# Performance work log

Hardware: AMD Instinct MI355X
Metric: run time of the kernel (lower is better)

The kernel has to match this reference:

```python
import jax, jax.numpy as jnp
import numpy as np

N_EXPERTS = 16
DS_DIM = 3

def _conv2d(x, w):
    # x: [B,C,H,W], w: [O,I,kH,kW], VALID, stride 1
    return jax.lax.conv_general_dilated(x, w, (1, 1), 'VALID',
                                        dimension_numbers=('NCHW', 'OIHW', 'NCHW'))

def _maxpool2(x):
    return jax.lax.reduce_window(x, -jnp.inf, jax.lax.max,
                                 (1, 1, 2, 2), (1, 1, 2, 2), 'VALID')

def _forward(x, conv1_w, conv1_b, conv2_w, conv2_b,
             fc1_w, fc1_b, fc2_w, fc2_b, fc3_w, fc3_b,
             fc4_w, fc4_b, fc5_w, fc5_b, B_mats, C_mats, x_tar):
    bsz = x.shape[0]
    img = x[:, DS_DIM:].reshape(bsz, 1, 64, 64)
    h = _maxpool2(jax.nn.relu(_conv2d(img, conv1_w) + conv1_b[None, :, None, None]))
    h = _maxpool2(jax.nn.relu(_conv2d(h, conv2_w) + conv2_b[None, :, None, None]))
    h = h.reshape(bsz, -1)                      # [B, 1690]
    h = jnp.concatenate([h, x[:, :DS_DIM]], axis=1)  # [B, 1693]
    h = jax.nn.relu(h @ fc1_w.T + fc1_b)
    h = jax.nn.relu(h @ fc2_w.T + fc2_b)
    h = jax.nn.relu(h @ fc3_w.T + fc3_b)
    h = jax.nn.relu(h @ fc4_w.T + fc4_b)
    w_all = jax.nn.softmax(h @ fc5_w.T + fc5_b, axis=1)   # [B, N]
    A = B_mats + C_mats                          # [N, d, d]
    diff = x_tar - x[:, :DS_DIM]                 # [B, d]
    # torch: sum_i w[:,i,None] * (A_i @ diff.T).T == einsum over experts
    s_all = jnp.einsum('bn,nij,bj->bi', w_all, A, diff)
    return s_all


def setup_inputs() -> dict:
    key = jax.random.key(0)
    ks = jax.random.split(key, 20)
    rn = lambda k, shp, s: jax.random.normal(k, shp, dtype=jnp.float32) * s
    d = {}
    d['x'] = rn(ks[0], (8192, 4099), 1.0)
    d['conv1_w'] = rn(ks[1], (5, 1, 5, 5), 0.2)
    d['conv1_b'] = rn(ks[2], (5,), 0.05)
    d['conv2_w'] = rn(ks[3], (10, 5, 5, 5), 0.09)
    d['conv2_b'] = rn(ks[4], (10,), 0.05)
    d['fc1_w'] = rn(ks[5], (512, 1693), 1.0 / np.sqrt(1693))
    d['fc1_b'] = rn(ks[6], (512,), 0.02)
    d['fc2_w'] = rn(ks[7], (256, 512), 1.0 / np.sqrt(512))
    d['fc2_b'] = rn(ks[8], (256,), 0.02)
    d['fc3_w'] = rn(ks[9], (128, 256), 1.0 / np.sqrt(256))
    d['fc3_b'] = rn(ks[10], (128,), 0.02)
    d['fc4_w'] = rn(ks[11], (64, 128), 1.0 / np.sqrt(128))
    d['fc4_b'] = rn(ks[12], (64,), 0.02)
    d['fc5_w'] = rn(ks[13], (N_EXPERTS, 64), 1.0 / np.sqrt(64))
    d['fc5_b'] = rn(ks[14], (N_EXPERTS,), 0.02)
    # geotorch constrains B to PSD and C to skew-symmetric; build such mats
    G = rn(ks[15], (N_EXPERTS, DS_DIM, DS_DIM), 0.5)
    d['B_mats'] = jnp.einsum('nij,nkj->nik', G, G)        # PSD
    S = rn(ks[16], (N_EXPERTS, DS_DIM, DS_DIM), 0.5)
    d['C_mats'] = S - jnp.swapaxes(S, 1, 2)               # skew
    d['x_tar'] = jnp.zeros((1, DS_DIM), dtype=jnp.float32)
    return d


def reference(x, conv1_w, conv1_b, conv2_w, conv2_b,
              fc1_w, fc1_b, fc2_w, fc2_b, fc3_w, fc3_b,
              fc4_w, fc4_b, fc5_w, fc5_b, B_mats, C_mats, x_tar):
    return _forward(x, conv1_w, conv1_b, conv2_w, conv2_b,
                    fc1_w, fc1_b, fc2_w, fc2_b, fc3_w, fc3_b,
                    fc4_w, fc4_b, fc5_w, fc5_b, B_mats, C_mats, x_tar)
```

## Files before the change

kernel.cpp:

```cpp
#include <hip/hip_runtime.h>
#include <hip/hip_bf16.h>
#include <hip/hip_fp16.h>
#include <math.h>

#define XW 4099
#define DSD 3
#define BSZ 8192
#define KP1 1696

typedef __attribute__((ext_vector_type(8))) _Float16 f16x8;
typedef __attribute__((ext_vector_type(4))) float    f32x4;

static __device__ __forceinline__ short f2h(float f) {
    union { _Float16 h; short s; } u;
    u.h = (_Float16)f;
    return u.s;
}

__global__ __launch_bounds__(256) void cvt_f16_pad(
    const float* __restrict__ src, short* __restrict__ dst,
    int N, int K, int Kp)
{
    const int tot = N * Kp;
    for (int i = blockIdx.x * 256 + threadIdx.x; i < tot; i += gridDim.x * 256) {
        const int n = i / Kp, k = i % Kp;
        dst[i] = (k < K) ? f2h(src[(size_t)n * K + k]) : (short)0;
    }
}

__global__ __launch_bounds__(256, 4) void conv_fused(
    const float* __restrict__ x,
    const float* __restrict__ w1, const float* __restrict__ b1,
    const float* __restrict__ w2, const float* __restrict__ b2,
    short* __restrict__ act1)
{
    __shared__ __align__(16) char smem0[64 * 68 * 4];
    float     (*img)[68]  = (float(*)[68])smem0;
    _Float16  (*w2f)[224] = (_Float16(*)[224])smem0;

    __shared__ __align__(16) _Float16  h1[30][30][8];
    __shared__ __align__(16) float     cw1[5][28];
    __shared__ float cb1[5];
    __shared__ float cb2s[16];
    __shared__ __align__(16) int kofft[28];

    const int b = blockIdx.x;
    const int t = threadIdx.x;

    const float* xr = x + (size_t)b * XW + DSD;
    #pragma unroll
    for (int i = 0; i < 16; ++i) {
        const int idx = t + 256 * i;
        img[idx >> 6][idx & 63] = xr[idx];
    }
    {
        uint4* h1z = (uint4*)&h1[0][0][0];
        const uint4 z4 = {0u, 0u, 0u, 0u};
        #pragma unroll
        for (int i = 0; i < 4; ++i) {
            const int idx = t + 256 * i;
            if (idx < 900) h1z[idx] = z4;
        }
    }
    if (t < 140) { const int c = t / 28, k = t % 28; cw1[c][k] = (k < 25) ? w1[c * 25 + k] : 0.f; }
    if (t >= 144 && t < 149) cb1[t - 144] = b1[t - 144];
    if (t >= 160 && t < 176) cb2s[t - 160] = (t - 160 < 10) ? b2[t - 160] : 0.f;
    if (t >= 192 && t < 220) {
        const int p = t - 192;
        kofft[p] = (p < 25) ? (p / 5) * 480 + (p % 5) * 16 : 0;
    }
    __syncthreads();

    if (t < 225) {
        const int ty = t / 15, tx = t % 15;
        const int y0 = 4 * ty, x0 = 4 * tx;
        f32x4 pv[8][2];
        #pragma unroll
        for (int r = 0; r < 8; ++r) {
            pv[r][0] = *(const f32x4*)&img[y0 + r][x0];
            pv[r][1] = *(const f32x4*)&img[y0 + r][x0 + 4];
        }
        asm volatile("" :
            "+v"(pv[0][0]), "+v"(pv[0][1]), "+v"(pv[1][0]), "+v"(pv[1][1]),
            "+v"(pv[2][0]), "+v"(pv[2][1]), "+v"(pv[3][0]), "+v"(pv[3][1]),
            "+v"(pv[4][0]), "+v"(pv[4][1]), "+v"(pv[5][0]), "+v"(pv[5][1]),
            "+v"(pv[6][0]), "+v"(pv[6][1]), "+v"(pv[7][0]), "+v"(pv[7][1]));
        #pragma unroll 1
        for (int c = 0; c < 5; ++c) {
            f32x4 wv4[7];
            #pragma unroll
            for (int i = 0; i < 7; ++i) wv4[i] = *(const f32x4*)&cw1[c][4 * i];
            const float bias = cb1[c];
            float acc[4][4];
            #pragma unroll
            for (int cy = 0; cy < 4; ++cy)
                #pragma unroll
                for (int cx = 0; cx < 4; ++cx) acc[cy][cx] = bias;
            #pragma unroll
            for (int ky = 0; ky < 5; ++ky)
                #pragma unroll
                for (int kx = 0; kx < 5; ++kx) {
                    const int kk = ky * 5 + kx;
                    const float wv = wv4[kk >> 2][kk & 3];
                    #pragma unroll
                    for (int cy = 0; cy < 4; ++cy)
                        #pragma unroll
                        for (int cx = 0; cx < 4; ++cx) {
                            const int px = cx + kx;
                            acc[cy][cx] += pv[cy + ky][px >> 2][px & 3] * wv;
                        }
                }
            #pragma unroll
            for (int sy = 0; sy < 2; ++sy)
                #pragma unroll
                for (int sx = 0; sx < 2; ++sx) {
                    const float m = fmaxf(
                        fmaxf(acc[2 * sy][2 * sx],     acc[2 * sy][2 * sx + 1]),
                        fmaxf(acc[2 * sy + 1][2 * sx], acc[2 * sy + 1][2 * sx + 1]));
                    h1[2 * ty + sy][2 * tx + sx][c] = (_Float16)fmaxf(m, 0.f);
                }
        }
    }
    __syncthreads();

    for (int i = t; i < 448; i += 256) {
        const int wc = i / 28, wp = i % 28;
        f16x8 cell;
        #pragma unroll
        for (int ic = 0; ic < 8; ++ic) cell[ic] = (_Float16)0.f;
        if (wc < 10 && wp < 25) {
            #pragma unroll
            for (int ic = 0; ic < 5; ++ic)
                cell[ic] = (_Float16)w2[(wc * 5 + ic) * 25 + wp];
        }
        *(f16x8*)&w2f[wc][wp * 8] = cell;
    }
    __syncthreads();

    short* outr = act1 + (size_t)b * KP1;
    {
        const int wv_ = t >> 6, lane = t & 63;
        const int lr = lane & 15, kg = lane >> 4;
        const float bias2 = cb2s[lr];
        const int qa = lr & 3;
        const int wa_off = lr >> 2;

        int bases[11];
        #pragma unroll
        for (int u = 0; u < 11; ++u) {
            const int tt = u * 4 + wv_;
            int w_A = tt * 4 + wa_off;
            w_A = (w_A < 169) ? w_A : 168;
            const int Y = (w_A * 5042) >> 16;
            const int X = w_A - Y * 13;
            bases[u] = (2 * Y + (qa & 1)) * 480 + (2 * X + (qa >> 1)) * 16;
        }

        f32x4 acc[11];
        #pragma unroll
        for (int u = 0; u < 11; ++u) acc[u] = (f32x4){0.f, 0.f, 0.f, 0.f};

        const char* h1p = (const char*)&h1[0][0][0];

        #pragma unroll 1
        for (int s = 0; s < 7; ++s) {
            const int koffp = kofft[s * 4 + kg];
            const f16x8 bfs = *(const f16x8*)&w2f[lr][s * 32 + kg * 8];
            #pragma unroll
            for (int u = 0; u < 11; ++u) {
                const f16x8 af = *(const f16x8*)(h1p + (bases[u] + koffp));
                acc[u] = __builtin_amdgcn_mfma_f32_16x16x32_f16(af, bfs, acc[u], 0, 0, 0);
            }
        }

        #pragma unroll
        for (int u = 0; u < 11; ++u) {
            const int tt = u * 4 + wv_;
            const int w_C = tt * 4 + kg;
            if (lr < 10 && w_C < 169) {
                const float m = fmaxf(fmaxf(acc[u][0], acc[u][1]), fmaxf(acc[u][2], acc[u][3]));
                outr[lr * 169 + w_C] = f2h(fmaxf(m + bias2, 0.f));
            }
        }
    }
    if (t < DSD)           outr[1690 + t] = f2h(x[(size_t)b * XW + t]);
    if (t >= DSD && t < 6) outr[1690 + t] = 0;
}

template <int RELU, int OUTH>
__global__ __launch_bounds__(256) void mfma_fc(
    const short* __restrict__ A,
    const short* __restrict__ W,
    const float* __restrict__ bias,
    void* __restrict__ Cout,
    int N, int Kp)
{
    __shared__ __align__(16) short As[64][40];
    __shared__ __align__(16) short Ws[64][40];

    const int tid  = threadIdx.x;
    const int m0   = blockIdx.y * 64;
    const int n0   = blockIdx.x * 64;
    const int wv   = tid >> 6, lane = tid & 63;
    const int rm   = (wv >> 1) * 32, rn = (wv & 1) * 32;
    const int lr   = lane & 15, kg = lane >> 4;
    const int sr   = tid >> 2, sc = (tid & 3) * 8;

    f32x4 acc[2][2];
    #pragma unroll
    for (int i = 0; i < 2; ++i)
        #pragma unroll
        for (int j = 0; j < 2; ++j)
            #pragma unroll
            for (int q = 0; q < 4; ++q) acc[i][j][q] = 0.f;

    for (int k0 = 0; k0 < Kp; k0 += 32) {
        *(uint4*)&As[sr][sc] = *(const uint4*)&A[(size_t)(m0 + sr) * Kp + k0 + sc];
        *(uint4*)&Ws[sr][sc] = *(const uint4*)&W[(size_t)(n0 + sr) * Kp + k0 + sc];
        __syncthreads();
        f16x8 aF[2], bF[2];
        #pragma unroll
        for (int mi = 0; mi < 2; ++mi) aF[mi] = *(const f16x8*)&As[rm + mi * 16 + lr][kg * 8];
        #pragma unroll
        for (int nj = 0; nj < 2; ++nj) bF[nj] = *(const f16x8*)&Ws[rn + nj * 16 + lr][kg * 8];
        #pragma unroll
        for (int mi = 0; mi < 2; ++mi)
            #pragma unroll
            for (int nj = 0; nj < 2; ++nj)
                acc[mi][nj] = __builtin_amdgcn_mfma_f32_16x16x32_f16(
                    aF[mi], bF[nj], acc[mi][nj], 0, 0, 0);
        __syncthreads();
    }

    #pragma unroll
    for (int mi = 0; mi < 2; ++mi)
        #pragma unroll
        for (int nj = 0; nj < 2; ++nj) {
            const int col  = n0 + rn + nj * 16 + lr;
            const int rowb = m0 + rm + mi * 16 + kg * 4;
            const float bv = bias[col];
            #pragma unroll
            for (int q = 0; q < 4; ++q) {
                float v = acc[mi][nj][q] + bv;
                if (RELU) v = fmaxf(v, 0.f);
                if (OUTH) ((short*)Cout)[(size_t)(rowb + q) * N + col] = f2h(v);
                else      ((float*)Cout)[(size_t)(rowb + q) * N + col] = v;
            }
        }
}

__global__ __launch_bounds__(256) void head_kernel(
    const float* __restrict__ act5, const float* __restrict__ w5,
    const float* __restrict__ b5, const float* __restrict__ Bm,
    const float* __restrict__ Cm, const float* __restrict__ x,
    const float* __restrict__ x_tar, float* __restrict__ out)
{
    __shared__ float sw[16 * 64];
    __shared__ float sb[16];
    __shared__ float sA[16 * 9];
    __shared__ float st[3];
    const int t = threadIdx.x;
    for (int i = t; i < 1024; i += 256) sw[i] = w5[i];
    if (t < 16)  sb[t] = b5[t];
    if (t < 144) sA[t] = Bm[t] + Cm[t];
    if (t < 3)   st[t] = x_tar[t];
    __syncthreads();

    const int b = blockIdx.x * 256 + t;
    float h[64];
    const float* ar = act5 + (size_t)b * 64;
    #pragma unroll
    for (int i = 0; i < 64; ++i) h[i] = ar[i];

    float logit[16];
    float mx = -1e30f;
    #pragma unroll
    for (int n = 0; n < 16; ++n) {
        float s = sb[n];
        const float* wr = sw + n * 64;
        #pragma unroll
        for (int i = 0; i < 64; ++i) s += h[i] * wr[i];
        logit[n] = s;
        mx = fmaxf(mx, s);
    }
    float sum = 0.f;
    #pragma unroll
    for (int n = 0; n < 16; ++n) { logit[n] = __expf(logit[n] - mx); sum += logit[n]; }
    const float inv = 1.f / sum;

    const float d0 = st[0] - x[(size_t)b * XW + 0];
    const float d1 = st[1] - x[(size_t)b * XW + 1];
    const float d2 = st[2] - x[(size_t)b * XW + 2];
    float s0 = 0.f, s1 = 0.f, s2 = 0.f;
    #pragma unroll
    for (int n = 0; n < 16; ++n) {
        const float w = logit[n] * inv;
        const float* An = sA + n * 9;
        s0 += w * (An[0] * d0 + An[1] * d1 + An[2] * d2);
        s1 += w * (An[3] * d0 + An[4] * d1 + An[5] * d2);
        s2 += w * (An[6] * d0 + An[7] * d1 + An[8] * d2);
    }
    out[(size_t)b * 3 + 0] = s0;
    out[(size_t)b * 3 + 1] = s1;
    out[(size_t)b * 3 + 2] = s2;
}

extern "C" void kernel_launch(void* const* d_in, const int* in_sizes, int n_in,
                              void* d_out, int out_size, void* d_ws, size_t ws_size,
                              hipStream_t stream) {
    const float* x       = (const float*)d_in[0];
    const float* conv1_w = (const float*)d_in[1];
    const float* conv1_b = (const float*)d_in[2];
    const float* conv2_w = (const float*)d_in[3];
    const float* conv2_b = (const float*)d_in[4];
    const float* fc1_w   = (const float*)d_in[5];
    const float* fc1_b   = (const float*)d_in[6];
    const float* fc2_w   = (const float*)d_in[7];
    const float* fc2_b   = (const float*)d_in[8];
    const float* fc3_w   = (const float*)d_in[9];
    const float* fc3_b   = (const float*)d_in[10];
    const float* fc4_w   = (const float*)d_in[11];
    const float* fc4_b   = (const float*)d_in[12];
    const float* fc5_w   = (const float*)d_in[13];
    const float* fc5_b   = (const float*)d_in[14];
    const float* B_mats  = (const float*)d_in[15];
    const float* C_mats  = (const float*)d_in[16];
    const float* x_tar   = (const float*)d_in[17];
    float* out = (float*)d_out;

    char* p = (char*)d_ws;
    short* act1 = (short*)p;  p += (size_t)BSZ * KP1 * 2;
    short* act2 = (short*)p;  p += (size_t)BSZ * 512 * 2;
    short* act3 = (short*)p;  p += (size_t)BSZ * 256 * 2;
    short* act4 = (short*)p;  p += (size_t)BSZ * 128 * 2;
    float* act5 = (float*)p;  p += (size_t)BSZ * 64 * 4;
    short* w1h  = (short*)p;  p += (size_t)512 * KP1 * 2;
    short* w2h  = (short*)p;  p += (size_t)256 * 512 * 2;
    short* w3h  = (short*)p;  p += (size_t)128 * 256 * 2;
    short* w4h  = (short*)p;  p += (size_t)64 * 128 * 2;

    cvt_f16_pad<<<1024, 256, 0, stream>>>(fc1_w, w1h, 512, 1693, KP1);
    cvt_f16_pad<<<256,  256, 0, stream>>>(fc2_w, w2h, 256, 512, 512);
    cvt_f16_pad<<<64,   256, 0, stream>>>(fc3_w, w3h, 128, 256, 256);
    cvt_f16_pad<<<16,   256, 0, stream>>>(fc4_w, w4h, 64, 128, 128);

    conv_fused<<<BSZ, 256, 0, stream>>>(x, conv1_w, conv1_b, conv2_w, conv2_b, act1);

    mfma_fc<1, 1><<<dim3(512 / 64, BSZ / 64), 256, 0, stream>>>(act1, w1h, fc1_b, act2, 512, KP1);
    mfma_fc<1, 1><<<dim3(256 / 64, BSZ / 64), 256, 0, stream>>>(act2, w2h, fc2_b, act3, 256, 512);
    mfma_fc<1, 1><<<dim3(128 / 64, BSZ / 64), 256, 0, stream>>>(act3, w3h, fc3_b, act4, 128, 256);
    mfma_fc<1, 0><<<dim3(64 / 64,  BSZ / 64), 256, 0, stream>>>(act4, w4h, fc4_b, act5, 64, 128);

    head_kernel<<<BSZ / 256, 256, 0, stream>>>(act5, fc5_w, fc5_b, B_mats, C_mats, x, x_tar, out);
}
```

Before: 218.2 us.

## Split conv1 into half-row passes and use 128-row tiles for fc1 GEMM

```diff
diff --git a/kernel.cpp b/kernel.cpp
--- a/kernel.cpp
+++ b/kernel.cpp
@@ -39,8 +39,6 @@
     _Float16  (*w2f)[224] = (_Float16(*)[224])smem0;
 
     __shared__ __align__(16) _Float16  h1[30][30][8];
-    __shared__ __align__(16) float     cw1[5][28];
-    __shared__ float cb1[5];
     __shared__ float cb2s[16];
     __shared__ __align__(16) int kofft[28];
 
@@ -62,8 +60,6 @@
             if (idx < 900) h1z[idx] = z4;
         }
     }
-    if (t < 140) { const int c = t / 28, k = t % 28; cw1[c][k] = (k < 25) ? w1[c * 25 + k] : 0.f; }
-    if (t >= 144 && t < 149) cb1[t - 144] = b1[t - 144];
     if (t >= 160 && t < 176) cb2s[t - 160] = (t - 160 < 10) ? b2[t - 160] : 0.f;
     if (t >= 192 && t < 220) {
         const int p = t - 192;
@@ -74,51 +70,43 @@
     if (t < 225) {
         const int ty = t / 15, tx = t % 15;
         const int y0 = 4 * ty, x0 = 4 * tx;
-        f32x4 pv[8][2];
-        #pragma unroll
-        for (int r = 0; r < 8; ++r) {
-            pv[r][0] = *(const f32x4*)&img[y0 + r][x0];
-            pv[r][1] = *(const f32x4*)&img[y0 + r][x0 + 4];
-        }
-        asm volatile("" :
-            "+v"(pv[0][0]), "+v"(pv[0][1]), "+v"(pv[1][0]), "+v"(pv[1][1]),
-            "+v"(pv[2][0]), "+v"(pv[2][1]), "+v"(pv[3][0]), "+v"(pv[3][1]),
-            "+v"(pv[4][0]), "+v"(pv[4][1]), "+v"(pv[5][0]), "+v"(pv[5][1]),
-            "+v"(pv[6][0]), "+v"(pv[6][1]), "+v"(pv[7][0]), "+v"(pv[7][1]));
         #pragma unroll 1
-        for (int c = 0; c < 5; ++c) {
-            f32x4 wv4[7];
-            #pragma unroll
-            for (int i = 0; i < 7; ++i) wv4[i] = *(const f32x4*)&cw1[c][4 * i];
-            const float bias = cb1[c];
-            float acc[4][4];
-            #pragma unroll
-            for (int cy = 0; cy < 4; ++cy)
+        for (int h = 0; h < 2; ++h) {
+            f32x4 pv[6][2];
+            #pragma unroll
+            for (int r = 0; r < 6; ++r) {
+                pv[r][0] = *(const f32x4*)&img[y0 + 2 * h + r][x0];
+                pv[r][1] = *(const f32x4*)&img[y0 + 2 * h + r][x0 + 4];
+            }
+            #pragma unroll 1
+            for (int c = 0; c < 5; ++c) {
+                const float bias = b1[c];
+                float acc[2][4];
                 #pragma unroll
-                for (int cx = 0; cx < 4; ++cx) acc[cy][cx] = bias;
-            #pragma unroll
-            for (int ky = 0; ky < 5; ++ky)
+                for (int cy = 0; cy < 2; ++cy)
+                    #pragma unroll
+                    for (int cx = 0; cx < 4; ++cx) acc[cy][cx] = bias;
                 #pragma unroll
-                for (int kx = 0; kx < 5; ++kx) {
-                    const int kk = ky * 5 + kx;
-                    const float wv = wv4[kk >> 2][kk & 3];
+                for (int ky = 0; ky < 5; ++ky)
                     #pragma unroll
-                    for (int cy = 0; cy < 4; ++cy)
+                    for (int kx = 0; kx < 5; ++kx) {
+                        const float wv = w1[c * 25 + ky * 5 + kx];
                         #pragma unroll
-                        for (int cx = 0; cx < 4; ++cx) {
-                            const int px = cx + kx;
-                            acc[cy][cx] += pv[cy + ky][px >> 2][px & 3] * wv;
-                        }
-                }
-            #pragma unroll
-            for (int sy = 0; sy < 2; ++sy)
+                        for (int cy = 0; cy < 2; ++cy)
+                            #pragma unroll
+                            for (int cx = 0; cx < 4; ++cx) {
+                                const int px = cx + kx;
+                                acc[cy][cx] += pv[cy + ky][px >> 2][px & 3] * wv;
+                            }
+                    }
                 #pragma unroll
                 for (int sx = 0; sx < 2; ++sx) {
                     const float m = fmaxf(
-                        fmaxf(acc[2 * sy][2 * sx],     acc[2 * sy][2 * sx + 1]),
-                        fmaxf(acc[2 * sy + 1][2 * sx], acc[2 * sy + 1][2 * sx + 1]));
-                    h1[2 * ty + sy][2 * tx + sx][c] = (_Float16)fmaxf(m, 0.f);
+                        fmaxf(acc[0][2 * sx], acc[0][2 * sx + 1]),
+                        fmaxf(acc[1][2 * sx], acc[1][2 * sx + 1]));
+                    h1[2 * ty + h][2 * tx + sx][c] = (_Float16)fmaxf(m, 0.f);
                 }
+            }
         }
     }
     __syncthreads();
@@ -189,10 +177,8 @@
 
 template <int RELU, int OUTH>
 __global__ __launch_bounds__(256) void mfma_fc(
-    const short* __restrict__ A,
-    const short* __restrict__ W,
-    const float* __restrict__ bias,
-    void* __restrict__ Cout,
+    const short* __restrict__ A, const short* __restrict__ W,
+    const float* __restrict__ bias, void* __restrict__ Cout,
     int N, int Kp)
 {
     __shared__ __align__(16) short As[64][40];
@@ -234,6 +220,68 @@
 
     #pragma unroll
     for (int mi = 0; mi < 2; ++mi)
+        #pragma unroll
+        for (int nj = 0; nj < 2; ++nj) {
+            const int col  = n0 + rn + nj * 16 + lr;
+            const int rowb = m0 + rm + mi * 16 + kg * 4;
+            const float bv = bias[col];
+            #pragma unroll
+            for (int q = 0; q < 4; ++q) {
+                float v = acc[mi][nj][q] + bv;
+                if (RELU) v = fmaxf(v, 0.f);
+                if (OUTH) ((short*)Cout)[(size_t)(rowb + q) * N + col] = f2h(v);
+                else      ((float*)Cout)[(size_t)(rowb + q) * N + col] = v;
+            }
+        }
+}
+
+template <int RELU, int OUTH>
+__global__ __launch_bounds__(256) void mfma_fc_big(
+    const short* __restrict__ A, const short* __restrict__ W,
+    const float* __restrict__ bias, void* __restrict__ Cout,
+    int N, int Kp)
+{
+    __shared__ __align__(16) short As[128][40];
+    __shared__ __align__(16) short Ws[64][40];
+
+    const int tid  = threadIdx.x;
+    const int m0   = blockIdx.y * 128;
+    const int n0   = blockIdx.x * 64;
+    const int wv   = tid >> 6, lane = tid & 63;
+    const int rm   = (wv >> 1) * 64, rn = (wv & 1) * 32;
+    const int lr   = lane & 15, kg = lane >> 4;
+    const int sa_r = tid >> 1, sa_c = (tid & 1) * 16;
+    const int sb_r = tid >> 2, sb_c = (tid & 3) * 8;
+
+    f32x4 acc[4][2];
+    #pragma unroll
+    for (int i = 0; i < 4; ++i)
+        #pragma unroll
+        for (int j = 0; j < 2; ++j)
+            #pragma unroll
+            for (int q = 0; q < 4; ++q) acc[i][j][q] = 0.f;
+
+    for (int k0 = 0; k0 < Kp; k0 += 32) {
+        *(uint4*)&As[sa_r][sa_c]     = *(const uint4*)&A[(size_t)(m0 + sa_r) * Kp + k0 + sa_c];
+        *(uint4*)&As[sa_r][sa_c + 8] = *(const uint4*)&A[(size_t)(m0 + sa_r) * Kp + k0 + sa_c + 8];
+        *(uint4*)&Ws[sb_r][sb_c]     = *(const uint4*)&W[(size_t)(n0 + sb_r) * Kp + k0 + sb_c];
+        __syncthreads();
+        f16x8 aF[4], bF[2];
+        #pragma unroll
+        for (int mi = 0; mi < 4; ++mi) aF[mi] = *(const f16x8*)&As[rm + mi * 16 + lr][kg * 8];
+        #pragma unroll
+        for (int nj = 0; nj < 2; ++nj) bF[nj] = *(const f16x8*)&Ws[rn + nj * 16 + lr][kg * 8];
+        #pragma unroll
+        for (int mi = 0; mi < 4; ++mi)
+            #pragma unroll
+            for (int nj = 0; nj < 2; ++nj)
+                acc[mi][nj] = __builtin_amdgcn_mfma_f32_16x16x32_f16(
+                    aF[mi], bF[nj], acc[mi][nj], 0, 0, 0);
+        __syncthreads();
+    }
+
+    #pragma unroll
+    for (int mi = 0; mi < 4; ++mi)
         #pragma unroll
         for (int nj = 0; nj < 2; ++nj) {
             const int col  = n0 + rn + nj * 16 + lr;
@@ -346,7 +394,7 @@
 
     conv_fused<<<BSZ, 256, 0, stream>>>(x, conv1_w, conv1_b, conv2_w, conv2_b, act1);
 
-    mfma_fc<1, 1><<<dim3(512 / 64, BSZ / 64), 256, 0, stream>>>(act1, w1h, fc1_b, act2, 512, KP1);
+    mfma_fc_big<1, 1><<<dim3(512 / 64, BSZ / 128), 256, 0, stream>>>(act1, w1h, fc1_b, act2, 512, KP1);
     mfma_fc<1, 1><<<dim3(256 / 64, BSZ / 64), 256, 0, stream>>>(act2, w2h, fc2_b, act3, 256, 512);
     mfma_fc<1, 1><<<dim3(128 / 64, BSZ / 64), 256, 0, stream>>>(act3, w3h, fc3_b, act4, 128, 256);
     mfma_fc<1, 0><<<dim3(64 / 64,  BSZ / 64), 256, 0, stream>>>(act4, w4h, fc4_b, act5, 64, 128);
```

Measured after the change: 241.4 us. +10.6%, slower.
